# Performance work log

Hardware: AMD Instinct MI355X
Metric: run time of the kernel (lower is better)

## Reference

```python
import jax, jax.numpy as jnp
import numpy as np

D = 256; NH = 8; HD = D // NH; L = 4; P = 4; NQ = 900; BS = 8; DFFN = 1024
SHAPES = np.array([[128, 128], [64, 64], [32, 32], [16, 16]])  # (H, W) per level, static metadata
NV = int((SHAPES[:, 0] * SHAPES[:, 1]).sum())
EPS = 1e-6


def setup_inputs():
    key = jax.random.key(0)
    ks = iter(jax.random.split(key, 48))

    def nrm(shape, scale=0.02):
        return jax.random.normal(next(ks), shape, jnp.float32) * scale

    lsi = np.concatenate([[0], np.cumsum(SHAPES[:, 0] * SHAPES[:, 1])[:-1]]).astype(np.int64)
    return {
        'tgt': nrm((NQ, BS, D), 1.0),
        'tgt_query_pos': nrm((NQ, BS, D), 1.0),
        'tgt_reference_points': jax.random.uniform(next(ks), (NQ, BS, L, 2), jnp.float32),
        'memory': nrm((NV, BS, D), 1.0),
        'memory_spatial_shapes': jnp.asarray(SHAPES, jnp.int32),
        'memory_level_start_index': jnp.asarray(lsi, jnp.int32),
        'w_norm_sa': jnp.ones((D,), jnp.float32),
        'w_norm_ca': jnp.ones((D,), jnp.float32),
        'w_norm_ffn': jnp.ones((D,), jnp.float32),
        'ls_sa': jnp.full((D,), 1e-4, jnp.float32),
        'ls_ca': jnp.full((D,), 1e-4, jnp.float32),
        'ls_ffn': jnp.full((D,), 1e-4, jnp.float32),
        'Wq': nrm((D, D)), 'Wk': nrm((D, D)), 'Wv': nrm((D, D)),
        'bq': jnp.zeros((D,), jnp.float32), 'bk': jnp.zeros((D,), jnp.float32), 'bv': jnp.zeros((D,), jnp.float32),
        'Wo_sa': nrm((D, D)), 'bo_sa': jnp.zeros((D,), jnp.float32),
        'Wv_proj': nrm((D, D)), 'bv_proj': jnp.zeros((D,), jnp.float32),
        'W_off': nrm((NH * L * P * 2, D)), 'b_off': nrm((NH * L * P * 2,), 0.1),
        'W_attn': nrm((NH * L * P, D)), 'b_attn': jnp.zeros((NH * L * P,), jnp.float32),
        'W_out_ca': nrm((D, D)), 'bo_ca': jnp.zeros((D,), jnp.float32),
        'Wg': nrm((DFFN, D)), 'bg': jnp.zeros((DFFN,), jnp.float32),
        'Wu': nrm((DFFN, D)), 'bu': jnp.zeros((DFFN,), jnp.float32),
        'Wf': nrm((D, DFFN)), 'bf': jnp.zeros((D,), jnp.float32),
    }


def rmsnorm(x, w):
    return x * jax.lax.rsqrt(jnp.mean(x * x, axis=-1, keepdims=True) + EPS) * w


def ms_deform_sample(v, loc, attw):
    # v: (bs, nv, NH, HD); loc: (bs, nq, NH, L, P, 2) normalized (x, y); attw: (bs, nq, NH, L, P)
    bs, nq = loc.shape[0], loc.shape[1]
    out = jnp.zeros((bs, nq, NH, HD), loc.dtype)
    b_idx = jnp.arange(bs)[:, None, None, None]
    h_idx = jnp.arange(NH)[None, None, :, None]
    start = 0
    for l in range(L):
        Hl, Wl = int(SHAPES[l, 0]), int(SHAPES[l, 1])
        vf = v[:, start:start + Hl * Wl]  # (bs, Hl*Wl, NH, HD)
        start += Hl * Wl
        # grid_sample(align_corners=False, padding=zeros) pixel mapping
        x = loc[:, :, :, l, :, 0] * Wl - 0.5
        y = loc[:, :, :, l, :, 1] * Hl - 0.5
        x0 = jnp.floor(x)
        y0 = jnp.floor(y)
        acc = jnp.zeros((bs, nq, NH, P, HD), loc.dtype)
        for dx in (0, 1):
            for dy in (0, 1):
                xi = x0 + dx
                yi = y0 + dy
                w = (1.0 - jnp.abs(x - xi)) * (1.0 - jnp.abs(y - yi))
                valid = (xi >= 0) & (xi <= Wl - 1) & (yi >= 0) & (yi <= Hl - 1)
                w = jnp.where(valid, w, 0.0)
                idx = (jnp.clip(yi, 0, Hl - 1) * Wl + jnp.clip(xi, 0, Wl - 1)).astype(jnp.int32)
                acc = acc + w[..., None] * vf[b_idx, idx, h_idx]  # (bs, nq, NH, P, HD)
        out = out + jnp.einsum('bqhp,bqhpd->bqhd', attw[:, :, :, l], acc)
    return out


def reference(tgt, tgt_query_pos, tgt_reference_points, memory, memory_spatial_shapes,
              memory_level_start_index, w_norm_sa, w_norm_ca, w_norm_ffn, ls_sa, ls_ca, ls_ffn,
              Wq, Wk, Wv, bq, bk, bv, Wo_sa, bo_sa, Wv_proj, bv_proj, W_off, b_off, W_attn,
              b_attn, W_out_ca, bo_ca, Wg, bg, Wu, bu, Wf, bf):
    nq, bs, d = tgt.shape
    # --- self-attention (pre-norm + LayerScale residual) ---
    xn = rmsnorm(tgt, w_norm_sa)
    qk = xn + tgt_query_pos
    q = (qk @ Wq.T + bq).reshape(nq, bs, NH, HD)
    k = (qk @ Wk.T + bk).reshape(nq, bs, NH, HD)
    vv = (xn @ Wv.T + bv).reshape(nq, bs, NH, HD)
    scores = jnp.einsum('qbhd,kbhd->bhqk', q, k) * (1.0 / np.sqrt(HD))
    attn = jax.nn.softmax(scores, axis=-1)
    sa = jnp.einsum('bhqk,kbhd->qbhd', attn, vv).reshape(nq, bs, d) @ Wo_sa.T + bo_sa
    tgt = tgt + ls_sa * sa
    # --- multi-scale deformable cross-attention (identity=zeros in original) ---
    xn = rmsnorm(tgt, w_norm_ca)
    qca = jnp.swapaxes(xn + tgt_query_pos, 0, 1)  # (bs, nq, d)
    val = (jnp.swapaxes(memory, 0, 1) @ Wv_proj.T + bv_proj).reshape(bs, -1, NH, HD)
    off = (qca @ W_off.T + b_off).reshape(bs, nq, NH, L, P, 2)
    attw = jax.nn.softmax((qca @ W_attn.T + b_attn).reshape(bs, nq, NH, L * P), axis=-1)
    attw = attw.reshape(bs, nq, NH, L, P)
    norm = jnp.asarray(SHAPES[:, ::-1].copy(), jnp.float32)  # (W, H) per level
    ref = jnp.swapaxes(tgt_reference_points, 0, 1)  # (bs, nq, L, 2)
    loc = ref[:, :, None, :, None, :] + off / norm[None, None, None, :, None, :]
    ca = ms_deform_sample(val, loc, attw).reshape(bs, nq, d) @ W_out_ca.T + bo_ca
    tgt = tgt + ls_ca * jnp.swapaxes(ca, 0, 1)
    # --- SwiGLU FFN ---
    xn = rmsnorm(tgt, w_norm_ffn)
    ffn = (jax.nn.silu(xn @ Wg.T + bg) * (xn @ Wu.T + bu)) @ Wf.T + bf
    return tgt + ls_ffn * ffn
```

## Files before the change

kernel.cpp:

```cpp
#include <hip/hip_runtime.h>

typedef unsigned short ushort_t;
typedef unsigned int uint32;
typedef __bf16 bf16x8 __attribute__((ext_vector_type(8)));
typedef float f32x4 __attribute__((ext_vector_type(4)));
typedef ushort_t us4 __attribute__((ext_vector_type(4)));

#define D_    256
#define NH_   8
#define HD_   32
#define NQ_   900
#define BS_   8
#define TOK_  7200
#define NV_   21760
#define QP_   928
#define DFFN_ 1024

__device__ __forceinline__ ushort_t f2bf(float x) {
    union { float f; uint32 u; } v; v.f = x;
    uint32 r = v.u + 0x7FFFu + ((v.u >> 16) & 1u);
    return (ushort_t)(r >> 16);
}
__device__ __forceinline__ float bf2f(ushort_t h) {
    union { uint32 u; float f; } v; v.u = ((uint32)h) << 16;
    return v.f;
}
__device__ __forceinline__ int imin(int a, int b) { return a < b ? a : b; }
__device__ __forceinline__ int imax(int a, int b) { return a > b ? a : b; }

__global__ __launch_bounds__(256) void cvtall_k(
    const float* __restrict__ s0, const float* __restrict__ s1, const float* __restrict__ s2,
    const float* __restrict__ s3, const float* __restrict__ s4, const float* __restrict__ s5,
    const float* __restrict__ s6, const float* __restrict__ s7, const float* __restrict__ s8,
    const float* __restrict__ s9, const float* __restrict__ s10, ushort_t* __restrict__ dst) {
    int id = blockIdx.x * 256 + threadIdx.x;
    const float* s; int off;
    if      (id <  16384) { s = s0;  off = id; }
    else if (id <  32768) { s = s1;  off = id - 16384; }
    else if (id <  49152) { s = s2;  off = id - 32768; }
    else if (id <  65536) { s = s3;  off = id - 49152; }
    else if (id <  81920) { s = s4;  off = id - 65536; }
    else if (id <  98304) { s = s5;  off = id - 81920; }
    else if (id < 114688) { s = s6;  off = id - 98304; }
    else if (id < 122880) { s = s7;  off = id - 114688; }
    else if (id < 188416) { s = s8;  off = id - 122880; }
    else if (id < 253952) { s = s9;  off = id - 188416; }
    else                  { s = s10; off = id - 253952; }
    f32x4 v = *(const f32x4*)(s + (size_t)off * 4);
    us4 t;
#pragma unroll
    for (int e = 0; e < 4; e++) t[e] = f2bf(v[e]);
    *(us4*)(dst + (size_t)id * 4) = t;
}

__global__ __launch_bounds__(256) void rms_k(const float* __restrict__ x,
                                             const float* __restrict__ pos,
                                             const float* __restrict__ wn,
                                             ushort_t* __restrict__ xn_out,
                                             ushort_t* __restrict__ qk_out) {
    int r = blockIdx.x, tid = threadIdx.x;
    float v = x[r * D_ + tid];
    float ss = v * v;
#pragma unroll
    for (int o = 32; o; o >>= 1) ss += __shfl_xor(ss, o, 64);
    __shared__ float part[4];
    if ((tid & 63) == 0) part[tid >> 6] = ss;
    __syncthreads();
    float tot = part[0] + part[1] + part[2] + part[3];
    float sc = rsqrtf(tot * (1.f / 256.f) + 1e-6f);
    float xn = v * sc * wn[tid];
    if (xn_out) xn_out[r * D_ + tid] = f2bf(xn);
    if (qk_out) qk_out[r * D_ + tid] = f2bf(xn + pos[r * D_ + tid]);
}

enum { EPI_BF16, EPI_F32, EPI_RESID, EPI_QK, EPI_VT, EPI_SILU };

template <int EPI, bool AF32, int BM, int BN, int WGM, int WGN, int TK>
__global__ __launch_bounds__(WGM * WGN * 64) void gemm2_k(
    const void* __restrict__ Ap, const ushort_t* __restrict__ Wp,
    const float* __restrict__ bias, void* __restrict__ outp,
    int M, int N, int swz,
    const float* __restrict__ resid, const float* __restrict__ ls,
    const float* __restrict__ gbuf, float scale) {
    constexpr int THREADS = WGM * WGN * 64;
    constexpr int NK  = TK / 32;
    constexpr int LDK = 40;
    constexpr int WR  = BM / WGM, WC = BN / WGN;
    constexpr int FM  = WR / 16,  FN = WC / 16;
    constexpr int ACH = AF32 ? (BM * 32 / 4 / THREADS) : (BM * 32 / 8 / THREADS);
    constexpr int BCH = BN * 32 / 8 / THREADS;

    __shared__ __align__(16) ushort_t As[2][BM * LDK];
    __shared__ __align__(16) ushort_t Bs[2][BN * LDK];

    const int tid = threadIdx.x, l = tid & 63, w = tid >> 6;
    const int wm = w % WGM, wn = w / WGM;
    int by = blockIdx.y;
    if (swz) { int cpx = gridDim.y >> 3; by = (by & 7) * cpx + (by >> 3); }
    const int m0 = by * BM, n0 = blockIdx.x * BN;
    const int lr = l & 15, lkb = (l >> 4) * 8;

    const ushort_t* Ab = (const ushort_t*)Ap;
    const float*    Af = (const float*)Ap;

    int aRow[ACH], aK[ACH], bRow[BCH], bK[BCH];
#pragma unroll
    for (int ch = 0; ch < ACH; ch++) {
        int cid = ch * THREADS + tid;
        if constexpr (AF32) { aRow[ch] = cid >> 3; aK[ch] = (cid & 7) * 4; }
        else                { aRow[ch] = cid >> 2; aK[ch] = (cid & 3) * 8; }
    }
#pragma unroll
    for (int ch = 0; ch < BCH; ch++) {
        int cid = ch * THREADS + tid;
        bRow[ch] = cid >> 2; bK[ch] = (cid & 3) * 8;
    }
    int aGRow[ACH];
#pragma unroll
    for (int ch = 0; ch < ACH; ch++) aGRow[ch] = imin(m0 + aRow[ch], M - 1);

    f32x4  aSTf[AF32 ? ACH : 1];
    bf16x8 aSTb[AF32 ? 1 : ACH];
    bf16x8 bST[BCH];

    auto load_regs = [&](int kt) {
        const int k0 = kt * 32;
#pragma unroll
        for (int ch = 0; ch < ACH; ch++) {
            if constexpr (AF32)
                aSTf[ch] = *(const f32x4*)(Af + (size_t)aGRow[ch] * TK + k0 + aK[ch]);
            else
                aSTb[ch] = *(const bf16x8*)(Ab + (size_t)aGRow[ch] * TK + k0 + aK[ch]);
        }
#pragma unroll
        for (int ch = 0; ch < BCH; ch++)
            bST[ch] = *(const bf16x8*)(Wp + (size_t)(n0 + bRow[ch]) * TK + k0 + bK[ch]);
    };
    auto write_lds = [&](int buf) {
#pragma unroll
        for (int ch = 0; ch < ACH; ch++) {
            if constexpr (AF32) {
                us4 t;
#pragma unroll
                for (int e = 0; e < 4; e++) t[e] = f2bf(aSTf[ch][e]);
                *(us4*)&As[buf][aRow[ch] * LDK + aK[ch]] = t;
            } else {
                *(bf16x8*)&As[buf][aRow[ch] * LDK + aK[ch]] = aSTb[ch];
            }
        }
#pragma unroll
        for (int ch = 0; ch < BCH; ch++)
            *(bf16x8*)&Bs[buf][bRow[ch] * LDK + bK[ch]] = bST[ch];
    };

    f32x4 acc[FM][FN];
#pragma unroll
    for (int i = 0; i < FM; i++)
#pragma unroll
        for (int j = 0; j < FN; j++) acc[i][j] = f32x4{0.f, 0.f, 0.f, 0.f};

    load_regs(0);
    write_lds(0);
    __syncthreads();

    for (int kt = 0; kt < NK; ++kt) {
        const int c = kt & 1;
        if (kt + 1 < NK) load_regs(kt + 1);

        bf16x8 af[FM], bf_[FN];
#pragma unroll
        for (int i = 0; i < FM; i++)
            af[i] = *(const bf16x8*)&As[c][(wm * WR + i * 16 + lr) * LDK + lkb];
#pragma unroll
        for (int j = 0; j < FN; j++)
            bf_[j] = *(const bf16x8*)&Bs[c][(wn * WC + j * 16 + lr) * LDK + lkb];
#pragma unroll
        for (int i = 0; i < FM; i++)
#pragma unroll
            for (int j = 0; j < FN; j++)
                acc[i][j] = __builtin_amdgcn_mfma_f32_16x16x32_bf16(af[i], bf_[j], acc[i][j], 0, 0, 0);

        if (kt + 1 < NK) write_lds(c ^ 1);
        __syncthreads();
    }

#pragma unroll
    for (int i = 0; i < FM; i++)
#pragma unroll
        for (int j = 0; j < FN; j++) {
            int col = n0 + wn * WC + j * 16 + lr;
            float bvv = bias[col];
#pragma unroll
            for (int e = 0; e < 4; e++) {
                int row = m0 + wm * WR + i * 16 + (l >> 4) * 4 + e;
                if (row >= M) continue;
                float v = acc[i][j][e] + bvv;
                if constexpr (EPI == EPI_BF16) {
                    ((ushort_t*)outp)[(size_t)row * N + col] = f2bf(v);
                } else if constexpr (EPI == EPI_F32) {
                    ((float*)outp)[(size_t)row * N + col] = v;
                } else if constexpr (EPI == EPI_RESID) {
                    size_t idx = (size_t)row * N + col;
                    ((float*)outp)[idx] = resid[idx] + ls[col] * v;
                } else if constexpr (EPI == EPI_QK) {
                    int q = row >> 3, bb = row & 7, h = col >> 5, hd = col & 31;
                    ((ushort_t*)outp)[((bb * NH_ + h) * QP_ + q) * HD_ + hd] = f2bf(v * scale);
                } else if constexpr (EPI == EPI_VT) {
                    int q = row >> 3, bb = row & 7, h = col >> 5, hd = col & 31;
                    ((ushort_t*)outp)[((bb * NH_ + h) * HD_ + hd) * QP_ + q] = f2bf(v);
                } else if constexpr (EPI == EPI_SILU) {
                    size_t idx = (size_t)row * N + col;
                    float g = gbuf[idx];
                    float s = g / (1.f + __expf(-g));
                    ((ushort_t*)outp)[idx] = f2bf(s * v);
                }
            }
        }
}

__global__ __launch_bounds__(256) void attn2_k(const ushort_t* __restrict__ qb,
                                               const ushort_t* __restrict__ kb,
                                               const ushort_t* __restrict__ vtb,
                                               ushort_t* __restrict__ sab) {
    __shared__ __align__(16) ushort_t Pl[4][16 * 40];
    const int tid = threadIdx.x, l = tid & 63, w = tid >> 6;
    const int bh = blockIdx.y, b = bh >> 3, h = bh & 7;
    const int q0 = (blockIdx.x * 4 + w) * 16;
    if (q0 >= NQ_) return;
    const int q = l & 15, g = l >> 4;
    ushort_t* Pw = &Pl[w][0];

    const bf16x8 qf = *(const bf16x8*)(qb + ((size_t)bh * QP_ + q0 + q) * HD_ + g * 8);
    const ushort_t* kbase = kb + (size_t)bh * QP_ * HD_;
    const ushort_t* vbase = vtb + (size_t)bh * HD_ * QP_;

    f32x4 O0 = {0.f, 0.f, 0.f, 0.f}, O1 = {0.f, 0.f, 0.f, 0.f};
    float m = -1e30f, sl = 0.f;

    auto ldk = [&](int t, int u) {
        return *(const bf16x8*)(kbase + (size_t)(t * 32 + u * 16 + q) * HD_ + g * 8);
    };
    auto ldv = [&](int t, int dh) {
        return *(const bf16x8*)(vbase + (size_t)(dh * 16 + q) * QP_ + t * 32 + g * 8);
    };
    bf16x8 kA = ldk(0, 0), kB = ldk(0, 1), v0 = ldv(0, 0), v1 = ldv(0, 1);

    for (int t = 0; t < 29; ++t) {
        bf16x8 nkA, nkB, nv0, nv1;
        if (t < 28) { nkA = ldk(t + 1, 0); nkB = ldk(t + 1, 1); nv0 = ldv(t + 1, 0); nv1 = ldv(t + 1, 1); }
        const f32x4 z = {0.f, 0.f, 0.f, 0.f};
        f32x4 sA = __builtin_amdgcn_mfma_f32_16x16x32_bf16(kA, qf, z, 0, 0, 0);
        f32x4 sB = __builtin_amdgcn_mfma_f32_16x16x32_bf16(kB, qf, z, 0, 0, 0);
        if (t == 28) {
            int k0 = 896 + g * 4;
#pragma unroll
            for (int e = 0; e < 4; e++) {
                if (k0 + e >= NQ_)      sA[e] = -1e30f;
                if (k0 + 16 + e >= NQ_) sB[e] = -1e30f;
            }
        }
        float tm = fmaxf(fmaxf(fmaxf(sA[0], sA[1]), fmaxf(sA[2], sA[3])),
                         fmaxf(fmaxf(sB[0], sB[1]), fmaxf(sB[2], sB[3])));
        tm = fmaxf(tm, __shfl_xor(tm, 16, 64));
        tm = fmaxf(tm, __shfl_xor(tm, 32, 64));
        float mn = fmaxf(m, tm);
        float r = exp2f(m - mn);
        m = mn;
#pragma unroll
        for (int e = 0; e < 4; e++) { O0[e] *= r; O1[e] *= r; }
        float pA[4], pB[4], ps = 0.f;
#pragma unroll
        for (int e = 0; e < 4; e++) {
            pA[e] = exp2f(sA[e] - m); pB[e] = exp2f(sB[e] - m);
            ps += pA[e] + pB[e];
        }
        sl = sl * r + ps;
        uint32 a0, a1, b0, b1;
        asm("v_cvt_pk_bf16_f32 %0, %1, %2" : "=v"(a0) : "v"(pA[0]), "v"(pA[1]));
        asm("v_cvt_pk_bf16_f32 %0, %1, %2" : "=v"(a1) : "v"(pA[2]), "v"(pA[3]));
        asm("v_cvt_pk_bf16_f32 %0, %1, %2" : "=v"(b0) : "v"(pB[0]), "v"(pB[1]));
        asm("v_cvt_pk_bf16_f32 %0, %1, %2" : "=v"(b1) : "v"(pB[2]), "v"(pB[3]));
        { uint2 tt; tt.x = a0; tt.y = a1; *(uint2*)(Pw + q * 40 + g * 4) = tt; }
        { uint2 tt; tt.x = b0; tt.y = b1; *(uint2*)(Pw + q * 40 + 16 + g * 4) = tt; }
        bf16x8 pf = *(const bf16x8*)(Pw + q * 40 + g * 8);
        O0 = __builtin_amdgcn_mfma_f32_16x16x32_bf16(v0, pf, O0, 0, 0, 0);
        O1 = __builtin_amdgcn_mfma_f32_16x16x32_bf16(v1, pf, O1, 0, 0, 0);
        kA = nkA; kB = nkB; v0 = nv0; v1 = nv1;
    }

    sl += __shfl_xor(sl, 16, 64);
    sl += __shfl_xor(sl, 32, 64);
    float inv = 1.f / sl;
    int row_q = q0 + q;
    if (row_q < NQ_) {
        ushort_t* op = sab + ((size_t)row_q * BS_ + b) * D_ + h * HD_ + g * 4;
#pragma unroll
        for (int dh = 0; dh < 2; dh++) {
            f32x4 Ov = dh ? O1 : O0;
            float e0 = Ov[0] * inv, e1 = Ov[1] * inv, e2 = Ov[2] * inv, e3 = Ov[3] * inv;
            uint32 w0, w1;
            asm("v_cvt_pk_bf16_f32 %0, %1, %2" : "=v"(w0) : "v"(e0), "v"(e1));
            asm("v_cvt_pk_bf16_f32 %0, %1, %2" : "=v"(w1) : "v"(e2), "v"(e3));
            *(uint32*)(op + dh * 16) = w0;
            *(uint32*)(op + dh * 16 + 2) = w1;
        }
    }
}

__global__ __launch_bounds__(256) void deform_k(
    const float* __restrict__ offb, const float* __restrict__ logb,
    const float* __restrict__ refpts, const int* __restrict__ shapes,
    const int* __restrict__ lsi, const ushort_t* __restrict__ val,
    ushort_t* __restrict__ ca) {
    __shared__ float off_l[256];
    __shared__ float attw[128];
    const int r = blockIdx.x;
    const int b = r & 7;
    const int tid = threadIdx.x;

    off_l[tid] = offb[r * 256 + tid];
    if (tid < 128) {
        float lg = logb[r * 128 + tid];
        float m = lg;
#pragma unroll
        for (int o = 1; o < 16; o <<= 1) m = fmaxf(m, __shfl_xor(m, o, 16));
        float e = __expf(lg - m);
        float s = e;
#pragma unroll
        for (int o = 1; o < 16; o <<= 1) s += __shfl_xor(s, o, 16);
        attw[tid] = e / s;
    }
    __syncthreads();

    const int h = tid >> 5, d = tid & 31;
    float acc = 0.f;
#pragma unroll
    for (int lvl = 0; lvl < 4; lvl++) {
        const int H = shapes[lvl * 2], W = shapes[lvl * 2 + 1];
        const int base = lsi[lvl];
        const float refx = refpts[(r * 4 + lvl) * 2];
        const float refy = refpts[(r * 4 + lvl) * 2 + 1];
#pragma unroll
        for (int p = 0; p < 4; p++) {
            int oi = ((h * 4 + lvl) * 4 + p) * 2;
            float x = (refx + off_l[oi] / (float)W) * (float)W - 0.5f;
            float y = (refy + off_l[oi + 1] / (float)H) * (float)H - 0.5f;
            float x0 = floorf(x), y0 = floorf(y);
            float fx = x - x0, fy = y - y0;
            int ix = (int)x0, iy = (int)y0;
            float sval = 0.f;
#pragma unroll
            for (int dy = 0; dy <= 1; dy++)
#pragma unroll
                for (int dx = 0; dx <= 1; dx++) {
                    int xi = ix + dx, yi = iy + dy;
                    float wq = (dx ? fx : 1.f - fx) * (dy ? fy : 1.f - fy);
                    if (xi < 0 || xi >= W || yi < 0 || yi >= H) wq = 0.f;
                    int cx = imin(imax(xi, 0), W - 1), cy = imin(imax(yi, 0), H - 1);
                    float vv = bf2f(val[((base + cy * W + cx) * BS_ + b) * D_ + h * HD_ + d]);
                    sval += wq * vv;
                }
            acc += attw[h * 16 + lvl * 4 + p] * sval;
        }
    }
    ca[r * 256 + tid] = f2bf(acc);
}

extern "C" void kernel_launch(void* const* d_in, const int* in_sizes, int n_in,
                              void* d_out, int out_size, void* d_ws, size_t ws_size,
                              hipStream_t stream) {
    (void)in_sizes; (void)n_in; (void)out_size; (void)ws_size;
    const float* tgt    = (const float*)d_in[0];
    const float* qpos   = (const float*)d_in[1];
    const float* refp   = (const float*)d_in[2];
    const float* mem    = (const float*)d_in[3];
    const int*   shapes = (const int*)d_in[4];
    const int*   lsi    = (const int*)d_in[5];
    const float* wnsa   = (const float*)d_in[6];
    const float* wnca   = (const float*)d_in[7];
    const float* wnffn  = (const float*)d_in[8];
    const float* lssa   = (const float*)d_in[9];
    const float* lsca   = (const float*)d_in[10];
    const float* lsffn  = (const float*)d_in[11];
    const float* Wq = (const float*)d_in[12];
    const float* Wk = (const float*)d_in[13];
    const float* Wv = (const float*)d_in[14];
    const float* bq = (const float*)d_in[15];
    const float* bk = (const float*)d_in[16];
    const float* bvv = (const float*)d_in[17];
    const float* Wo_sa = (const float*)d_in[18];
    const float* bo_sa = (const float*)d_in[19];
    const float* Wv_proj = (const float*)d_in[20];
    const float* bv_proj = (const float*)d_in[21];
    const float* W_off = (const float*)d_in[22];
    const float* b_off = (const float*)d_in[23];
    const float* W_attn = (const float*)d_in[24];
    const float* b_attn = (const float*)d_in[25];
    const float* W_out = (const float*)d_in[26];
    const float* bo_ca = (const float*)d_in[27];
    const float* Wg = (const float*)d_in[28];
    const float* bg = (const float*)d_in[29];
    const float* Wu = (const float*)d_in[30];
    const float* bu = (const float*)d_in[31];
    const float* Wf = (const float*)d_in[32];
    const float* bff = (const float*)d_in[33];

    char* ws = (char*)d_ws;
    size_t o = 0;
    auto alloc = [&](size_t b) { size_t c = o; o += (b + 255) & ~(size_t)255; return c; };

    const size_t wq_o = alloc(65536 * 2), wk_o = alloc(65536 * 2), wv_o = alloc(65536 * 2);
    const size_t wosa_o = alloc(65536 * 2), wvp_o = alloc(65536 * 2), woff_o = alloc(65536 * 2);
    const size_t wout_o = alloc(65536 * 2), wattn_o = alloc(32768 * 2);
    const size_t wg_o = alloc(262144 * 2), wu_o = alloc(262144 * 2), wf_o = alloc(262144 * 2);
    const size_t xnsa_o = alloc((size_t)TOK_ * D_ * 2);
    const size_t qksa_o = alloc((size_t)TOK_ * D_ * 2);
    const size_t qkvBytes = (size_t)BS_ * NH_ * QP_ * HD_ * 2;
    const size_t qb_o = alloc(qkvBytes);
    const size_t kb_o = alloc(qkvBytes);
    const size_t vt_o = alloc(qkvBytes + 512);
    const size_t sa_o = alloc((size_t)TOK_ * D_ * 2);
    const size_t tgt1_o = alloc((size_t)TOK_ * D_ * 4);
    const size_t qca_o = alloc((size_t)TOK_ * D_ * 2);
    const size_t offb_o = alloc((size_t)TOK_ * 256 * 4);
    const size_t logit_o = alloc((size_t)TOK_ * 128 * 4);
    const size_t ca_o = alloc((size_t)TOK_ * D_ * 2);
    const size_t tgt2_o = alloc((size_t)TOK_ * D_ * 4);
    const size_t val_o = alloc((size_t)NV_ * BS_ * D_ * 2);
    const size_t g_o  = val_o;
    const size_t h_o  = val_o + (size_t)TOK_ * DFFN_ * 4;
    const size_t xn3_o = h_o + (size_t)TOK_ * DFFN_ * 2;

    dim3 blk(256);
    cvtall_k<<<dim3(319488 / 256), blk, 0, stream>>>(
        Wq, Wk, Wv, Wo_sa, Wv_proj, W_off, W_out, W_attn, Wg, Wu, Wf,
        (ushort_t*)(ws + wq_o));

    hipMemsetAsync(ws + qb_o, 0, qkvBytes, stream);
    hipMemsetAsync(ws + kb_o, 0, qkvBytes, stream);
    hipMemsetAsync(ws + vt_o, 0, qkvBytes + 512, stream);

    rms_k<<<dim3(TOK_), blk, 0, stream>>>(tgt, qpos, wnsa,
                                          (ushort_t*)(ws + xnsa_o), (ushort_t*)(ws + qksa_o));
    const float QSC = 0.25503321550239915f;
    gemm2_k<EPI_QK, false, 64, 128, 2, 2, 256><<<dim3(2, 113), blk, 0, stream>>>(
        ws + qksa_o, (ushort_t*)(ws + wq_o), bq, ws + qb_o, TOK_, 256, 0,
        nullptr, nullptr, nullptr, QSC);
    gemm2_k<EPI_QK, false, 64, 128, 2, 2, 256><<<dim3(2, 113), blk, 0, stream>>>(
        ws + qksa_o, (ushort_t*)(ws + wk_o), bk, ws + kb_o, TOK_, 256, 0,
        nullptr, nullptr, nullptr, 1.f);
    gemm2_k<EPI_VT, false, 64, 128, 2, 2, 256><<<dim3(2, 113), blk, 0, stream>>>(
        ws + xnsa_o, (ushort_t*)(ws + wv_o), bvv, ws + vt_o, TOK_, 256, 0,
        nullptr, nullptr, nullptr, 1.f);
    attn2_k<<<dim3(15, 64), blk, 0, stream>>>((ushort_t*)(ws + qb_o), (ushort_t*)(ws + kb_o),
                                              (ushort_t*)(ws + vt_o), (ushort_t*)(ws + sa_o));
    gemm2_k<EPI_RESID, false, 64, 128, 2, 2, 256><<<dim3(2, 113), blk, 0, stream>>>(
        ws + sa_o, (ushort_t*)(ws + wosa_o), bo_sa, ws + tgt1_o, TOK_, 256, 0,
        tgt, lssa, nullptr, 1.f);

    rms_k<<<dim3(TOK_), blk, 0, stream>>>((const float*)(ws + tgt1_o), qpos, wnca,
                                          nullptr, (ushort_t*)(ws + qca_o));
    gemm2_k<EPI_F32, false, 64, 128, 2, 2, 256><<<dim3(2, 113), blk, 0, stream>>>(
        ws + qca_o, (ushort_t*)(ws + woff_o), b_off, ws + offb_o, TOK_, 256, 0,
        nullptr, nullptr, nullptr, 1.f);
    gemm2_k<EPI_F32, false, 64, 128, 2, 2, 256><<<dim3(1, 113), blk, 0, stream>>>(
        ws + qca_o, (ushort_t*)(ws + wattn_o), b_attn, ws + logit_o, TOK_, 128, 0,
        nullptr, nullptr, nullptr, 1.f);
    gemm2_k<EPI_BF16, true, 128, 256, 2, 4, 256><<<dim3(1, 1360), dim3(512), 0, stream>>>(
        mem, (ushort_t*)(ws + wvp_o), bv_proj, ws + val_o, NV_ * BS_, 256, 1,
        nullptr, nullptr, nullptr, 1.f);
    deform_k<<<dim3(TOK_), blk, 0, stream>>>(
        (const float*)(ws + offb_o), (const float*)(ws + logit_o), refp, shapes, lsi,
        (ushort_t*)(ws + val_o), (ushort_t*)(ws + ca_o));
    gemm2_k<EPI_RESID, false, 64, 128, 2, 2, 256><<<dim3(2, 113), blk, 0, stream>>>(
        ws + ca_o, (ushort_t*)(ws + wout_o), bo_ca, ws + tgt2_o, TOK_, 256, 0,
        (const float*)(ws + tgt1_o), lsca, nullptr, 1.f);

    rms_k<<<dim3(TOK_), blk, 0, stream>>>((const float*)(ws + tgt2_o), nullptr, wnffn,
                                          (ushort_t*)(ws + xn3_o), nullptr);
    gemm2_k<EPI_F32, false, 128, 128, 2, 2, 256><<<dim3(8, 57), blk, 0, stream>>>(
        ws + xn3_o, (ushort_t*)(ws + wg_o), bg, ws + g_o, TOK_, 1024, 0,
        nullptr, nullptr, nullptr, 1.f);
    gemm2_k<EPI_SILU, false, 128, 128, 2, 2, 256><<<dim3(8, 57), blk, 0, stream>>>(
        ws + xn3_o, (ushort_t*)(ws + wu_o), bu, ws + h_o, TOK_, 1024, 0,
        nullptr, nullptr, (const float*)(ws + g_o), 1.f);
    gemm2_k<EPI_RESID, false, 64, 128, 2, 2, 1024><<<dim3(2, 113), blk, 0, stream>>>(
        ws + h_o, (ushort_t*)(ws + wf_o), bff, d_out, TOK_, 256, 0,
        (const float*)(ws + tgt2_o), lsffn, nullptr, 1.f);
}
```

Baseline: 379.2 us.

## Fuse QK, offset/logit and gate/up GEMMs; relayout value to head-major

Result: faster. 340.4 us (-10.2%).

```diff
diff --git a/kernel.cpp b/kernel.cpp
--- a/kernel.cpp
+++ b/kernel.cpp
@@ -32,8 +32,18 @@
     const float* __restrict__ s0, const float* __restrict__ s1, const float* __restrict__ s2,
     const float* __restrict__ s3, const float* __restrict__ s4, const float* __restrict__ s5,
     const float* __restrict__ s6, const float* __restrict__ s7, const float* __restrict__ s8,
-    const float* __restrict__ s9, const float* __restrict__ s10, ushort_t* __restrict__ dst) {
-    int id = blockIdx.x * 256 + threadIdx.x;
+    const float* __restrict__ s9, const float* __restrict__ s10, ushort_t* __restrict__ dst,
+    const float* __restrict__ bq, const float* __restrict__ bk,
+    const float* __restrict__ boff, const float* __restrict__ battn,
+    float* __restrict__ bias_qk, float* __restrict__ bias_ol) {
+    int tid = threadIdx.x;
+    if (blockIdx.x == 0) {
+        bias_qk[tid] = bq[tid];
+        bias_qk[256 + tid] = bk[tid];
+        bias_ol[tid] = boff[tid];
+        if (tid < 128) bias_ol[256 + tid] = battn[tid];
+    }
+    int id = blockIdx.x * 256 + tid;
     const float* s; int off;
     if      (id <  16384) { s = s0;  off = id; }
     else if (id <  32768) { s = s1;  off = id - 16384; }
@@ -73,15 +83,14 @@
     if (qk_out) qk_out[r * D_ + tid] = f2bf(xn + pos[r * D_ + tid]);
 }
 
-enum { EPI_BF16, EPI_F32, EPI_RESID, EPI_QK, EPI_VT, EPI_SILU };
+enum { EPI_RESID, EPI_QK2, EPI_VT, EPI_VAL, EPI_OFFLOG };
 
 template <int EPI, bool AF32, int BM, int BN, int WGM, int WGN, int TK>
 __global__ __launch_bounds__(WGM * WGN * 64) void gemm2_k(
     const void* __restrict__ Ap, const ushort_t* __restrict__ Wp,
-    const float* __restrict__ bias, void* __restrict__ outp,
+    const float* __restrict__ bias, void* __restrict__ outp, void* __restrict__ outp2,
     int M, int N, int swz,
-    const float* __restrict__ resid, const float* __restrict__ ls,
-    const float* __restrict__ gbuf, float scale) {
+    const float* __restrict__ resid, const float* __restrict__ ls, float scale) {
     constexpr int THREADS = WGM * WGN * 64;
     constexpr int NK  = TK / 32;
     constexpr int LDK = 40;
@@ -195,25 +204,117 @@
                 int row = m0 + wm * WR + i * 16 + (l >> 4) * 4 + e;
                 if (row >= M) continue;
                 float v = acc[i][j][e] + bvv;
-                if constexpr (EPI == EPI_BF16) {
-                    ((ushort_t*)outp)[(size_t)row * N + col] = f2bf(v);
-                } else if constexpr (EPI == EPI_F32) {
-                    ((float*)outp)[(size_t)row * N + col] = v;
-                } else if constexpr (EPI == EPI_RESID) {
+                if constexpr (EPI == EPI_RESID) {
                     size_t idx = (size_t)row * N + col;
                     ((float*)outp)[idx] = resid[idx] + ls[col] * v;
-                } else if constexpr (EPI == EPI_QK) {
-                    int q = row >> 3, bb = row & 7, h = col >> 5, hd = col & 31;
-                    ((ushort_t*)outp)[((bb * NH_ + h) * QP_ + q) * HD_ + hd] = f2bf(v * scale);
+                } else if constexpr (EPI == EPI_QK2) {
+                    int c2 = col & 255;
+                    int q = row >> 3, bb = row & 7, h = c2 >> 5, hd = c2 & 31;
+                    ushort_t* dst = (col < 256) ? (ushort_t*)outp : (ushort_t*)outp2;
+                    float sc = (col < 256) ? scale : 1.f;
+                    dst[((bb * NH_ + h) * QP_ + q) * HD_ + hd] = f2bf(v * sc);
                 } else if constexpr (EPI == EPI_VT) {
                     int q = row >> 3, bb = row & 7, h = col >> 5, hd = col & 31;
                     ((ushort_t*)outp)[((bb * NH_ + h) * HD_ + hd) * QP_ + q] = f2bf(v);
-                } else if constexpr (EPI == EPI_SILU) {
-                    size_t idx = (size_t)row * N + col;
-                    float g = gbuf[idx];
-                    float s = g / (1.f + __expf(-g));
-                    ((ushort_t*)outp)[idx] = f2bf(s * v);
+                } else if constexpr (EPI == EPI_VAL) {
+                    int vv = row >> 3, bb = row & 7, h = col >> 5, d = col & 31;
+                    ((ushort_t*)outp)[(((size_t)(bb * NH_ + h)) * NV_ + vv) * HD_ + d] = f2bf(v);
+                } else if constexpr (EPI == EPI_OFFLOG) {
+                    if (col < 256) ((float*)outp)[(size_t)row * 256 + col] = v;
+                    else           ((float*)outp2)[(size_t)row * 128 + col - 256] = v;
                 }
+            }
+        }
+}
+
+__global__ __launch_bounds__(256) void ffn_k(
+    const ushort_t* __restrict__ Ap, const ushort_t* __restrict__ Wg,
+    const ushort_t* __restrict__ Wu, const float* __restrict__ bgp,
+    const float* __restrict__ bup, ushort_t* __restrict__ outp, int M) {
+    constexpr int BM = 64, BN = 128, TK = 256, NK = TK / 32, LDK = 40;
+    constexpr int WR = 32, WC = 64, FM = 2, FN = 4;
+
+    __shared__ __align__(16) ushort_t As[2][BM * LDK];
+    __shared__ __align__(16) ushort_t Gs[2][BN * LDK];
+    __shared__ __align__(16) ushort_t Us[2][BN * LDK];
+
+    const int tid = threadIdx.x, l = tid & 63, w = tid >> 6;
+    const int wm = w & 1, wn = w >> 1;
+    const int m0 = blockIdx.y * BM, n0 = blockIdx.x * BN;
+    const int lr = l & 15, lkb = (l >> 4) * 8;
+
+    const int aRow = tid >> 2, aK = (tid & 3) * 8;
+    int bRow[2], bK[2];
+#pragma unroll
+    for (int ch = 0; ch < 2; ch++) { int cid = ch * 256 + tid; bRow[ch] = cid >> 2; bK[ch] = (cid & 3) * 8; }
+    const int aGRow = imin(m0 + aRow, M - 1);
+
+    bf16x8 aST, gST[2], uST[2];
+    auto load_regs = [&](int kt) {
+        const int k0 = kt * 32;
+        aST = *(const bf16x8*)(Ap + (size_t)aGRow * TK + k0 + aK);
+#pragma unroll
+        for (int ch = 0; ch < 2; ch++) {
+            gST[ch] = *(const bf16x8*)(Wg + (size_t)(n0 + bRow[ch]) * TK + k0 + bK[ch]);
+            uST[ch] = *(const bf16x8*)(Wu + (size_t)(n0 + bRow[ch]) * TK + k0 + bK[ch]);
+        }
+    };
+    auto write_lds = [&](int buf) {
+        *(bf16x8*)&As[buf][aRow * LDK + aK] = aST;
+#pragma unroll
+        for (int ch = 0; ch < 2; ch++) {
+            *(bf16x8*)&Gs[buf][bRow[ch] * LDK + bK[ch]] = gST[ch];
+            *(bf16x8*)&Us[buf][bRow[ch] * LDK + bK[ch]] = uST[ch];
+        }
+    };
+
+    f32x4 accG[FM][FN], accU[FM][FN];
+#pragma unroll
+    for (int i = 0; i < FM; i++)
+#pragma unroll
+        for (int j = 0; j < FN; j++) { accG[i][j] = f32x4{0,0,0,0}; accU[i][j] = f32x4{0,0,0,0}; }
+
+    load_regs(0);
+    write_lds(0);
+    __syncthreads();
+
+    for (int kt = 0; kt < NK; ++kt) {
+        const int c = kt & 1;
+        if (kt + 1 < NK) load_regs(kt + 1);
+        bf16x8 af[FM], gf[FN], uf[FN];
+#pragma unroll
+        for (int i = 0; i < FM; i++)
+            af[i] = *(const bf16x8*)&As[c][(wm * WR + i * 16 + lr) * LDK + lkb];
+#pragma unroll
+        for (int j = 0; j < FN; j++) {
+            gf[j] = *(const bf16x8*)&Gs[c][(wn * WC + j * 16 + lr) * LDK + lkb];
+            uf[j] = *(const bf16x8*)&Us[c][(wn * WC + j * 16 + lr) * LDK + lkb];
+        }
+#pragma unroll
+        for (int i = 0; i < FM; i++)
+#pragma unroll
+            for (int j = 0; j < FN; j++) {
+                accG[i][j] = __builtin_amdgcn_mfma_f32_16x16x32_bf16(af[i], gf[j], accG[i][j], 0, 0, 0);
+                accU[i][j] = __builtin_amdgcn_mfma_f32_16x16x32_bf16(af[i], uf[j], accU[i][j], 0, 0, 0);
+            }
+        if (kt + 1 < NK) write_lds(c ^ 1);
+        __syncthreads();
+    }
+
+#pragma unroll
+    for (int i = 0; i < FM; i++)
+#pragma unroll
+        for (int j = 0; j < FN; j++) {
+            int col = n0 + wn * WC + j * 16 + lr;
+            float bg_ = bgp[col], bu_ = bup[col];
+#pragma unroll
+            for (int e = 0; e < 4; e++) {
+                int row = m0 + wm * WR + i * 16 + (l >> 4) * 4 + e;
+                if (row >= M) continue;
+                float g = accG[i][j][e] + bg_;
+                float u = accU[i][j][e] + bu_;
+                float s = g / (1.f + __expf(-g));
+                outp[(size_t)row * DFFN_ + col] = f2bf(s * u);
             }
         }
 }
@@ -318,9 +419,9 @@
     const int b = r & 7;
     const int tid = threadIdx.x;
 
-    off_l[tid] = offb[r * 256 + tid];
+    off_l[tid] = offb[(size_t)r * 256 + tid];
     if (tid < 128) {
-        float lg = logb[r * 128 + tid];
+        float lg = logb[(size_t)r * 128 + tid];
         float m = lg;
 #pragma unroll
         for (int o = 1; o < 16; o <<= 1) m = fmaxf(m, __shfl_xor(m, o, 16));
@@ -333,6 +434,7 @@
     __syncthreads();
 
     const int h = tid >> 5, d = tid & 31;
+    const ushort_t* vb = val + ((size_t)(b * NH_ + h)) * NV_ * HD_;
     float acc = 0.f;
 #pragma unroll
     for (int lvl = 0; lvl < 4; lvl++) {
@@ -357,13 +459,13 @@
                     float wq = (dx ? fx : 1.f - fx) * (dy ? fy : 1.f - fy);
                     if (xi < 0 || xi >= W || yi < 0 || yi >= H) wq = 0.f;
                     int cx = imin(imax(xi, 0), W - 1), cy = imin(imax(yi, 0), H - 1);
-                    float vv = bf2f(val[((base + cy * W + cx) * BS_ + b) * D_ + h * HD_ + d]);
+                    float vv = bf2f(vb[(size_t)(base + cy * W + cx) * HD_ + d]);
                     sval += wq * vv;
                 }
             acc += attw[h * 16 + lvl * 4 + p] * sval;
         }
     }
-    ca[r * 256 + tid] = f2bf(acc);
+    ca[(size_t)r * 256 + tid] = f2bf(acc);
 }
 
 extern "C" void kernel_launch(void* const* d_in, const int* in_sizes, int n_in,
@@ -410,9 +512,10 @@
     auto alloc = [&](size_t b) { size_t c = o; o += (b + 255) & ~(size_t)255; return c; };
 
     const size_t wq_o = alloc(65536 * 2), wk_o = alloc(65536 * 2), wv_o = alloc(65536 * 2);
-    const size_t wosa_o = alloc(65536 * 2), wvp_o = alloc(65536 * 2), woff_o = alloc(65536 * 2);
-    const size_t wout_o = alloc(65536 * 2), wattn_o = alloc(32768 * 2);
+    const size_t wosa_o = alloc(65536 * 2), wvp_o = alloc(65536 * 2), wout_o = alloc(65536 * 2);
+    const size_t woff_o = alloc(65536 * 2), wattn_o = alloc(32768 * 2);
     const size_t wg_o = alloc(262144 * 2), wu_o = alloc(262144 * 2), wf_o = alloc(262144 * 2);
+    const size_t bqk_o = alloc(512 * 4), bol_o = alloc(384 * 4);
     const size_t xnsa_o = alloc((size_t)TOK_ * D_ * 2);
     const size_t qksa_o = alloc((size_t)TOK_ * D_ * 2);
     const size_t qkvBytes = (size_t)BS_ * NH_ * QP_ * HD_ * 2;
@@ -427,64 +530,53 @@
     const size_t ca_o = alloc((size_t)TOK_ * D_ * 2);
     const size_t tgt2_o = alloc((size_t)TOK_ * D_ * 4);
     const size_t val_o = alloc((size_t)NV_ * BS_ * D_ * 2);
-    const size_t g_o  = val_o;
-    const size_t h_o  = val_o + (size_t)TOK_ * DFFN_ * 4;
+    const size_t h_o  = val_o;
     const size_t xn3_o = h_o + (size_t)TOK_ * DFFN_ * 2;
 
     dim3 blk(256);
     cvtall_k<<<dim3(319488 / 256), blk, 0, stream>>>(
-        Wq, Wk, Wv, Wo_sa, Wv_proj, W_off, W_out, W_attn, Wg, Wu, Wf,
-        (ushort_t*)(ws + wq_o));
-
-    hipMemsetAsync(ws + qb_o, 0, qkvBytes, stream);
-    hipMemsetAsync(ws + kb_o, 0, qkvBytes, stream);
-    hipMemsetAsync(ws + vt_o, 0, qkvBytes + 512, stream);
+        Wq, Wk, Wv, Wo_sa, Wv_proj, W_out, W_off, W_attn, Wg, Wu, Wf,
+        (ushort_t*)(ws + wq_o),
+        bq, bk, b_off, b_attn, (float*)(ws + bqk_o), (float*)(ws + bol_o));
+
+    (void)hipMemsetAsync(ws + vt_o, 0, qkvBytes + 512, stream);
 
     rms_k<<<dim3(TOK_), blk, 0, stream>>>(tgt, qpos, wnsa,
                                           (ushort_t*)(ws + xnsa_o), (ushort_t*)(ws + qksa_o));
     const float QSC = 0.25503321550239915f;
-    gemm2_k<EPI_QK, false, 64, 128, 2, 2, 256><<<dim3(2, 113), blk, 0, stream>>>(
-        ws + qksa_o, (ushort_t*)(ws + wq_o), bq, ws + qb_o, TOK_, 256, 0,
-        nullptr, nullptr, nullptr, QSC);
-    gemm2_k<EPI_QK, false, 64, 128, 2, 2, 256><<<dim3(2, 113), blk, 0, stream>>>(
-        ws + qksa_o, (ushort_t*)(ws + wk_o), bk, ws + kb_o, TOK_, 256, 0,
-        nullptr, nullptr, nullptr, 1.f);
+    gemm2_k<EPI_QK2, false, 64, 128, 2, 2, 256><<<dim3(4, 113), blk, 0, stream>>>(
+        ws + qksa_o, (ushort_t*)(ws + wq_o), (const float*)(ws + bqk_o),
+        ws + qb_o, ws + kb_o, TOK_, 512, 0, nullptr, nullptr, QSC);
     gemm2_k<EPI_VT, false, 64, 128, 2, 2, 256><<<dim3(2, 113), blk, 0, stream>>>(
-        ws + xnsa_o, (ushort_t*)(ws + wv_o), bvv, ws + vt_o, TOK_, 256, 0,
-        nullptr, nullptr, nullptr, 1.f);
+        ws + xnsa_o, (ushort_t*)(ws + wv_o), bvv, ws + vt_o, nullptr, TOK_, 256, 0,
+        nullptr, nullptr, 1.f);
     attn2_k<<<dim3(15, 64), blk, 0, stream>>>((ushort_t*)(ws + qb_o), (ushort_t*)(ws + kb_o),
                                               (ushort_t*)(ws + vt_o), (ushort_t*)(ws + sa_o));
     gemm2_k<EPI_RESID, false, 64, 128, 2, 2, 256><<<dim3(2, 113), blk, 0, stream>>>(
-        ws + sa_o, (ushort_t*)(ws + wosa_o), bo_sa, ws + tgt1_o, TOK_, 256, 0,
-        tgt, lssa, nullptr, 1.f);
+        ws + sa_o, (ushort_t*)(ws + wosa_o), bo_sa, ws + tgt1_o, nullptr, TOK_, 256, 0,
+        tgt, lssa, 1.f);
 
     rms_k<<<dim3(TOK_), blk, 0, stream>>>((const float*)(ws + tgt1_o), qpos, wnca,
                                           nullptr, (ushort_t*)(ws + qca_o));
-    gemm2_k<EPI_F32, false, 64, 128, 2, 2, 256><<<dim3(2, 113), blk, 0, stream>>>(
-        ws + qca_o, (ushort_t*)(ws + woff_o), b_off, ws + offb_o, TOK_, 256, 0,
-        nullptr, nullptr, nullptr, 1.f);
-    gemm2_k<EPI_F32, false, 64, 128, 2, 2, 256><<<dim3(1, 113), blk, 0, stream>>>(
-        ws + qca_o, (ushort_t*)(ws + wattn_o), b_attn, ws + logit_o, TOK_, 128, 0,
-        nullptr, nullptr, nullptr, 1.f);
-    gemm2_k<EPI_BF16, true, 128, 256, 2, 4, 256><<<dim3(1, 1360), dim3(512), 0, stream>>>(
-        mem, (ushort_t*)(ws + wvp_o), bv_proj, ws + val_o, NV_ * BS_, 256, 1,
-        nullptr, nullptr, nullptr, 1.f);
+    gemm2_k<EPI_OFFLOG, false, 64, 128, 2, 2, 256><<<dim3(3, 113), blk, 0, stream>>>(
+        ws + qca_o, (ushort_t*)(ws + woff_o), (const float*)(ws + bol_o),
+        ws + offb_o, ws + logit_o, TOK_, 384, 0, nullptr, nullptr, 1.f);
+    gemm2_k<EPI_VAL, true, 128, 256, 2, 4, 256><<<dim3(1, 1360), dim3(512), 0, stream>>>(
+        mem, (ushort_t*)(ws + wvp_o), bv_proj, ws + val_o, nullptr, NV_ * BS_, 256, 1,
+        nullptr, nullptr, 1.f);
     deform_k<<<dim3(TOK_), blk, 0, stream>>>(
         (const float*)(ws + offb_o), (const float*)(ws + logit_o), refp, shapes, lsi,
         (ushort_t*)(ws + val_o), (ushort_t*)(ws + ca_o));
     gemm2_k<EPI_RESID, false, 64, 128, 2, 2, 256><<<dim3(2, 113), blk, 0, stream>>>(
-        ws + ca_o, (ushort_t*)(ws + wout_o), bo_ca, ws + tgt2_o, TOK_, 256, 0,
-        (const float*)(ws + tgt1_o), lsca, nullptr, 1.f);
+        ws + ca_o, (ushort_t*)(ws + wout_o), bo_ca, ws + tgt2_o, nullptr, TOK_, 256, 0,
+        (const float*)(ws + tgt1_o), lsca, 1.f);
 
     rms_k<<<dim3(TOK_), blk, 0, stream>>>((const float*)(ws + tgt2_o), nullptr, wnffn,
                                           (ushort_t*)(ws + xn3_o), nullptr);
-    gemm2_k<EPI_F32, false, 128, 128, 2, 2, 256><<<dim3(8, 57), blk, 0, stream>>>(
-        ws + xn3_o, (ushort_t*)(ws + wg_o), bg, ws + g_o, TOK_, 1024, 0,
-        nullptr, nullptr, nullptr, 1.f);
-    gemm2_k<EPI_SILU, false, 128, 128, 2, 2, 256><<<dim3(8, 57), blk, 0, stream>>>(
-        ws + xn3_o, (ushort_t*)(ws + wu_o), bu, ws + h_o, TOK_, 1024, 0,
-        nullptr, nullptr, (const float*)(ws + g_o), 1.f);
+    ffn_k<<<dim3(8, 113), blk, 0, stream>>>(
+        (const ushort_t*)(ws + xn3_o), (const ushort_t*)(ws + wg_o),
+        (const ushort_t*)(ws + wu_o), bg, bu, (ushort_t*)(ws + h_o), TOK_);
     gemm2_k<EPI_RESID, false, 64, 128, 2, 2, 1024><<<dim3(2, 113), blk, 0, stream>>>(
-        ws + h_o, (ushort_t*)(ws + wf_o), bff, d_out, TOK_, 256, 0,
-        (const float*)(ws + tgt2_o), lsffn, nullptr, 1.f);
-}
+        ws + h_o, (ushort_t*)(ws + wf_o), bff, d_out, nullptr, TOK_, 256, 0,
+        (const float*)(ws + tgt2_o), lsffn, 1.f);
+}
```
